# Kernel optimization log

Hardware: AMD Instinct MI355X
Metric: run time of the kernel (lower is better)

## Reference

```python
import jax, jax.numpy as jnp
import numpy as np

H, W, SCALE = 480, 640, 8  # full-res grid and coarse downsample factor (hw0_i/hw0_c)


def _struct_feats(pts, anchor_ids):
    """pts: [N, H*W, 3]; anchor_ids: [N, A] int -> [N, L, 4*A] with L=(H//SCALE)*(W//SCALE)."""
    N = pts.shape[0]
    coarse = pts.reshape(N, H, W, 3)[:, ::SCALE, ::SCALE, :].reshape(N, -1, 3)  # [N, L, 3]
    anchors = jnp.take_along_axis(pts, anchor_ids[:, :, None], axis=1)          # [N, A, 3]
    diff = coarse[:, :, None, :] - anchors[:, None, :, :]                        # [N, L, A, 3]
    dist = jnp.sum(diff * diff, axis=-1, keepdims=True)                          # [N, L, A, 1]
    s = jnp.concatenate([diff, dist], axis=-1)                                   # [N, L, A, 4]
    s = s / jnp.sum(jnp.abs(s), axis=-2, keepdims=True)                          # L1 norm over anchor axis
    s = jnp.swapaxes(s, -1, -2).reshape(N, coarse.shape[1], -1)                  # [N, L, 4A]
    return s


def _mlp(x, W1, b1, W2, b2):
    return jax.nn.relu(x @ W1 + b1) @ W2 + b2


def setup_inputs() -> dict:
    key = jax.random.key(0)
    ks = jax.random.split(key, 10)
    N, L, C, A, P = 4, 4800, 256, 128, H * W
    D = C + 4 * A  # 768
    return {
        "feat0": jax.random.normal(ks[0], (N, L, C), jnp.float32),
        "feat1": jax.random.normal(ks[1], (N, L, C), jnp.float32),
        "pts_3d0": jax.random.normal(ks[2], (N, P, 3), jnp.float32),
        "pts_3d1": jax.random.normal(ks[3], (N, P, 3), jnp.float32),
        "anchor_i_ids": jax.random.randint(ks[4], (N, A), 0, P),
        "anchor_j_ids": jax.random.randint(ks[5], (N, A), 0, P),
        "W1": jax.random.normal(ks[6], (D, D), jnp.float32) * (1.0 / np.sqrt(D)),
        "b1": jnp.zeros((D,), jnp.float32),
        "W2": jax.random.normal(ks[7], (D, C), jnp.float32) * (1.0 / np.sqrt(D)),
        "b2": jnp.zeros((C,), jnp.float32),
    }


def reference(feat0, feat1, pts_3d0, pts_3d1, anchor_i_ids, anchor_j_ids, W1, b1, W2, b2):
    s0 = _struct_feats(pts_3d0, anchor_i_ids)  # [N, L, 4A]
    s1 = _struct_feats(pts_3d1, anchor_j_ids)
    aug0 = _mlp(jnp.concatenate([feat0, s0], axis=-1), W1, b1, W2, b2)  # [N, L, C]
    aug1 = _mlp(jnp.concatenate([feat1, s1], axis=-1), W1, b1, W2, b2)
    return (aug0, aug1)
```

## Files before the change

kernel.cpp:

```cpp
#include <hip/hip_runtime.h>
#include <stdint.h>
#include <stddef.h>

typedef __attribute__((ext_vector_type(8))) short short8;
typedef __attribute__((ext_vector_type(4))) short short4v;
typedef __attribute__((ext_vector_type(4))) float f32x4;

typedef const __attribute__((address_space(3))) char* lds_cp;

#define GLDS16(gp, lp)                                                        \
    __builtin_amdgcn_global_load_lds(                                         \
        (const __attribute__((address_space(1))) void*)(gp),                  \
        (__attribute__((address_space(3))) void*)(lp), 16, 0, 0)

__device__ __forceinline__ short8 ldsr16(lds_cp p) {
    short8 v;
    asm volatile("ds_read_b128 %0, %1" : "=v"(v) : "v"(p));
    return v;
}

template <int N>
__device__ __forceinline__ void wait_lgkm() {
    static_assert(N == 0 || N == 2 || N == 4 || N == 8, "unsupported count");
    if constexpr (N == 0) asm volatile("s_waitcnt lgkmcnt(0)" ::: "memory");
    else if constexpr (N == 2) asm volatile("s_waitcnt lgkmcnt(2)" ::: "memory");
    else if constexpr (N == 4) asm volatile("s_waitcnt lgkmcnt(4)" ::: "memory");
    else if constexpr (N == 8) asm volatile("s_waitcnt lgkmcnt(8)" ::: "memory");
    __builtin_amdgcn_sched_barrier(0);
}

__device__ __forceinline__ unsigned short f2bf(float f) {
    union { float f; uint32_t u; } v;
    v.f = f;
    uint32_t u = v.u;
    u += 0x7FFFu + ((u >> 16) & 1u);
    return (unsigned short)(u >> 16);
}

__global__ __launch_bounds__(1024) void transpose_to_bf16(
    const float* __restrict__ src, unsigned short* __restrict__ dst, int R, int C)
{
    __shared__ float tile[32][33];
    const int c0 = blockIdx.x * 32, r0 = blockIdx.y * 32;
    const int tx = threadIdx.x, ty = threadIdx.y;
    tile[ty][tx] = src[(size_t)(r0 + ty) * C + (c0 + tx)];
    __syncthreads();
    dst[(size_t)(c0 + ty) * R + (r0 + tx)] = f2bf(tile[tx][ty]);
}

__global__ __launch_bounds__(64) void struct_pack(
    const float* __restrict__ feat0, const float* __restrict__ feat1,
    const float* __restrict__ pts0,  const float* __restrict__ pts1,
    const int* __restrict__ ids0,    const int* __restrict__ ids1,
    unsigned short* __restrict__ xw)
{
    const int m = blockIdx.x;
    const int t = m / 19200;
    const int r = m % 19200;
    const int n = r / 4800;
    const int l = r % 4800;
    const float* feat = t ? feat1 : feat0;
    const float* pts  = (t ? pts1 : pts0) + (size_t)n * (307200 * 3);
    const int*   ids  = (t ? ids1 : ids0) + n * 128;
    const int a = threadIdx.x;

    const int lr = l / 80, lc = l % 80;
    const int p  = (lr * 8) * 640 + lc * 8;
    const float cx = pts[p * 3 + 0], cy = pts[p * 3 + 1], cz = pts[p * 3 + 2];

    const int id0 = ids[a], id1 = ids[a + 64];
    const float d0x = cx - pts[id0 * 3 + 0];
    const float d0y = cy - pts[id0 * 3 + 1];
    const float d0z = cz - pts[id0 * 3 + 2];
    const float d0d = d0x * d0x + d0y * d0y + d0z * d0z;
    const float d1x = cx - pts[id1 * 3 + 0];
    const float d1y = cy - pts[id1 * 3 + 1];
    const float d1z = cz - pts[id1 * 3 + 2];
    const float d1d = d1x * d1x + d1y * d1y + d1z * d1z;

    float p0 = fabsf(d0x) + fabsf(d1x);
    float p1 = fabsf(d0y) + fabsf(d1y);
    float p2 = fabsf(d0z) + fabsf(d1z);
    float p3 = d0d + d1d;
#pragma unroll
    for (int off = 32; off; off >>= 1) {
        p0 += __shfl_xor(p0, off);
        p1 += __shfl_xor(p1, off);
        p2 += __shfl_xor(p2, off);
        p3 += __shfl_xor(p3, off);
    }
    const float i0 = 1.0f / p0, i1 = 1.0f / p1, i2 = 1.0f / p2, i3 = 1.0f / p3;

    unsigned short* xrow = xw + (size_t)m * 768;
    const float* frow = feat + (size_t)(n * 4800 + l) * 256;
    const float4 fv = ((const float4*)frow)[a];
    short4v s4;
    s4.x = (short)f2bf(fv.x); s4.y = (short)f2bf(fv.y);
    s4.z = (short)f2bf(fv.z); s4.w = (short)f2bf(fv.w);
    *(short4v*)(xrow + a * 4) = s4;

    xrow[256 + 0 * 128 + a]      = f2bf(d0x * i0);
    xrow[256 + 0 * 128 + a + 64] = f2bf(d1x * i0);
    xrow[256 + 1 * 128 + a]      = f2bf(d0y * i1);
    xrow[256 + 1 * 128 + a + 64] = f2bf(d1y * i1);
    xrow[256 + 2 * 128 + a]      = f2bf(d0z * i2);
    xrow[256 + 2 * 128 + a + 64] = f2bf(d1z * i2);
    xrow[256 + 3 * 128 + a]      = f2bf(d0d * i3);
    xrow[256 + 3 * 128 + a + 64] = f2bf(d1d * i3);
}

template <int MI, int NJ, int WRN_LOG, bool RELU, bool OUT_BF16>
__global__ __launch_bounds__(512, 2) void gemm_t(
    const unsigned short* __restrict__ A,
    const unsigned short* __restrict__ Bt,
    const float* __restrict__ bias,
    void* __restrict__ Cout,
    int K, int N, int ntx, int q8, int r8)
{
    constexpr int WRN = 1 << WRN_LOG;
    constexpr int WRM = 8 / WRN;
    constexpr int BM = WRM * MI * 16;
    constexpr int BN = WRN * NJ * 16;
    constexpr int ASLOT = BM * 128;
    constexpr int BSLOT = BN * 128;
    constexpr int ALD = BM / 64;
    constexpr int BLD = BN / 64;
    static_assert(ALD == 4, "vmcnt immediates assume 4 A-loads/wave/tile");
    static_assert(MI + NJ <= 13, "lgkm in-flight cap");

    extern __shared__ char lds[];
    const int nt = K >> 6;

    const int bid = blockIdx.x;
    const int xcd = bid & 7, idx = bid >> 3;
    const int w = (xcd < r8 ? xcd * (q8 + 1) : r8 * (q8 + 1) + (xcd - r8) * q8) + idx;
    const int n0 = (w % ntx) * BN;
    const int m0 = (w / ntx) * BM;

    const int tid = threadIdx.x;
    const int lane = tid & 63;
    const int wv = tid >> 6;
    const int wr = wv >> WRN_LOG;
    const int wc = wv & (WRN - 1);

    const int slr = lane >> 3;
    const int kc  = (lane & 7) ^ slr;
    const unsigned short* gA = A  + (size_t)(m0 + wv * 8 + slr) * K + kc * 8;
    const unsigned short* gB = Bt + (size_t)(n0 + wv * 8 + slr) * K + kc * 8;

    auto stA = [&](int slot, int i, int kt) {
        GLDS16(gA + (size_t)i * 64 * K + kt, lds + slot * ASLOT + (i * 64 + wv * 8) * 128);
    };
    auto stB = [&](int slot, int j, int kt) {
        GLDS16(gB + (size_t)j * 64 * K + kt, lds + 3 * ASLOT + slot * BSLOT + (j * 64 + wv * 8) * 128);
    };

    const int rsel = lane & 15;
    const int kbh  = lane >> 4;
    const int ck0 = ((kbh) ^ (rsel & 7)) * 16;
    const int ck1 = ((4 + kbh) ^ (rsel & 7)) * 16;
    const int aRowB = (wr * (MI * 16) + rsel) * 128;
    const int bRowB = (wc * (NJ * 16) + rsel) * 128;

    auto LDA = [&](int slot, int mi, int ks) -> short8 {
        return ldsr16((lds_cp)(lds + slot * ASLOT + aRowB + mi * 2048 + (ks ? ck1 : ck0)));
    };
    auto LDB = [&](int slot, int nj, int ks) -> short8 {
        return ldsr16((lds_cp)(lds + 3 * ASLOT + slot * BSLOT + bRowB + nj * 2048 + (ks ? ck1 : ck0)));
    };

    f32x4 acc[MI][NJ] = {};
    short8 aL[MI / 2], aH[MI / 2], aL1[MI / 2], aH1[MI / 2], bF0[NJ], bF1[NJ];

    {
#pragma unroll
        for (int i = 0; i < ALD; ++i) stA(0, i, 0);
#pragma unroll
        for (int j = 0; j < BLD; ++j) stB(0, j, 0);
        if (nt > 1) {
#pragma unroll
            for (int i = 0; i < ALD; ++i) stA(1, i, 64);
            asm volatile("s_waitcnt vmcnt(4)" ::: "memory");
        } else {
            asm volatile("s_waitcnt vmcnt(0)" ::: "memory");
        }
        __builtin_amdgcn_s_barrier();
    }

    int cb3 = 0;
    for (int t = 0; t < nt; ++t) {
        const int cb2 = t & 1;
        const int sb2 = cb2 ^ 1;
        int sa3 = cb3 + 2; if (sa3 >= 3) sa3 -= 3;
        const int kt1 = (t + 1) << 6;
        const int kt2 = (t + 2) << 6;
        const bool stb = (t + 1) < nt;
        const bool sta = (t + 2) < nt;

#pragma unroll
        for (int nj = 0; nj < NJ; ++nj) bF0[nj] = LDB(cb2, nj, 0);
#pragma unroll
        for (int mi = 0; mi < MI / 2; ++mi) aL[mi] = LDA(cb3, mi, 0);
#pragma unroll
        for (int mi = 0; mi < MI / 2; ++mi) aH[mi] = LDA(cb3, MI / 2 + mi, 0);

        wait_lgkm<MI / 2>();
        __builtin_amdgcn_s_setprio(1);
#pragma unroll
        for (int mi = 0; mi < MI / 2; ++mi)
#pragma unroll
            for (int nj = 0; nj < NJ; ++nj)
                acc[mi][nj] = __builtin_amdgcn_mfma_f32_16x16x32_bf16(aL[mi], bF0[nj], acc[mi][nj], 0, 0, 0);
        __builtin_amdgcn_s_setprio(0);

#pragma unroll
        for (int nj = 0; nj < NJ; ++nj) bF1[nj] = LDB(cb2, nj, 1);
        if (stb) {
#pragma unroll
            for (int j = 0; j < BLD; ++j) stB(sb2, j, kt1);
        }

        wait_lgkm<NJ>();
        __builtin_amdgcn_s_setprio(1);
#pragma unroll
        for (int mi = 0; mi < MI / 2; ++mi)
#pragma unroll
            for (int nj = 0; nj < NJ; ++nj)
                acc[MI / 2 + mi][nj] = __builtin_amdgcn_mfma_f32_16x16x32_bf16(aH[mi], bF0[nj], acc[MI / 2 + mi][nj], 0, 0, 0);
        __builtin_amdgcn_s_setprio(0);

#pragma unroll
        for (int mi = 0; mi < MI / 2; ++mi) aL1[mi] = LDA(cb3, mi, 1);
#pragma unroll
        for (int mi = 0; mi < MI / 2; ++mi) aH1[mi] = LDA(cb3, MI / 2 + mi, 1);
        if (sta) {
            stA(sa3, 0, kt2); stA(sa3, 1, kt2); stA(sa3, 2, kt2); stA(sa3, 3, kt2);
        }

        wait_lgkm<MI / 2>();
        __builtin_amdgcn_s_setprio(1);
#pragma unroll
        for (int mi = 0; mi < MI / 2; ++mi)
#pragma unroll
            for (int nj = 0; nj < NJ; ++nj)
                acc[mi][nj] = __builtin_amdgcn_mfma_f32_16x16x32_bf16(aL1[mi], bF1[nj], acc[mi][nj], 0, 0, 0);
        __builtin_amdgcn_s_setprio(0);

        wait_lgkm<0>();
        __builtin_amdgcn_s_setprio(1);
#pragma unroll
        for (int mi = 0; mi < MI / 2; ++mi)
#pragma unroll
            for (int nj = 0; nj < NJ; ++nj)
                acc[MI / 2 + mi][nj] = __builtin_amdgcn_mfma_f32_16x16x32_bf16(aH1[mi], bF1[nj], acc[MI / 2 + mi][nj], 0, 0, 0);
        __builtin_amdgcn_s_setprio(0);

        if (t + 1 < nt) {
            if (sta) asm volatile("s_waitcnt vmcnt(4)" ::: "memory");
            else     asm volatile("s_waitcnt vmcnt(0)" ::: "memory");
            __builtin_amdgcn_s_barrier();
        }
        cb3 = (cb3 + 1 == 3) ? 0 : cb3 + 1;
    }

    const int crow = (lane >> 4) * 4;
    const int ccol = lane & 15;
#pragma unroll
    for (int nj = 0; nj < NJ; ++nj) {
        const int col = n0 + wc * (NJ * 16) + nj * 16 + ccol;
        const float bv = bias[col];
#pragma unroll
        for (int mi = 0; mi < MI; ++mi) {
#pragma unroll
            for (int rg = 0; rg < 4; ++rg) {
                const int row = m0 + wr * (MI * 16) + mi * 16 + crow + rg;
                float v = acc[mi][nj][rg] + bv;
                if (RELU) v = fmaxf(v, 0.0f);
                if (OUT_BF16) {
                    ((unsigned short*)Cout)[(size_t)row * N + col] = f2bf(v);
                } else {
                    ((float*)Cout)[(size_t)row * N + col] = v;
                }
            }
        }
    }
}

extern "C" void kernel_launch(void* const* d_in, const int* in_sizes, int n_in,
                              void* d_out, int out_size, void* d_ws, size_t ws_size,
                              hipStream_t stream) {
    const float* feat0 = (const float*)d_in[0];
    const float* feat1 = (const float*)d_in[1];
    const float* pts0  = (const float*)d_in[2];
    const float* pts1  = (const float*)d_in[3];
    const int*   ids0  = (const int*)d_in[4];
    const int*   ids1  = (const int*)d_in[5];
    const float* W1    = (const float*)d_in[6];
    const float* b1    = (const float*)d_in[7];
    const float* W2    = (const float*)d_in[8];
    const float* b2    = (const float*)d_in[9];
    float* out = (float*)d_out;

    char* ws = (char*)d_ws;
    unsigned short* xw  = (unsigned short*)(ws);
    unsigned short* h   = (unsigned short*)(ws + 58982400);
    unsigned short* w1t = (unsigned short*)(ws + 117964800);
    unsigned short* w2t = (unsigned short*)(ws + 119144448);

    const int LDS1 = 3 * 32768 + 2 * 32768;
    const int LDS2 = 3 * 32768 + 2 * 16384;
    (void)hipFuncSetAttribute((const void*)&gemm_t<8, 4, 2, true, true>,
                              hipFuncAttributeMaxDynamicSharedMemorySize, LDS1);
    (void)hipFuncSetAttribute((const void*)&gemm_t<4, 4, 1, false, false>,
                              hipFuncAttributeMaxDynamicSharedMemorySize, LDS2);

    dim3 tb(32, 32);
    transpose_to_bf16<<<dim3(768 / 32, 768 / 32), tb, 0, stream>>>(W1, w1t, 768, 768);
    transpose_to_bf16<<<dim3(256 / 32, 768 / 32), tb, 0, stream>>>(W2, w2t, 768, 256);

    struct_pack<<<38400, 64, 0, stream>>>(feat0, feat1, pts0, pts1, ids0, ids1, xw);

    gemm_t<8, 4, 2, true, true><<<450, 512, LDS1, stream>>>(xw, w1t, b1, (void*)h, 768, 768, 3, 56, 2);
    gemm_t<4, 4, 1, false, false><<<300, 512, LDS2, stream>>>(h, w2t, b2, (void*)out, 768, 256, 2, 37, 4);
}
```

Baseline: 116.9 us.

## Merge weight transposes, batch struct_pack rows, shrink second GEMM tile

```diff
diff --git a/kernel.cpp b/kernel.cpp
--- a/kernel.cpp
+++ b/kernel.cpp
@@ -29,6 +29,14 @@
     __builtin_amdgcn_sched_barrier(0);
 }
 
+template <int N>
+__device__ __forceinline__ void wait_vm() {
+    static_assert(N == 0 || N == 2 || N == 4, "unsupported count");
+    if constexpr (N == 0) asm volatile("s_waitcnt vmcnt(0)" ::: "memory");
+    else if constexpr (N == 2) asm volatile("s_waitcnt vmcnt(2)" ::: "memory");
+    else if constexpr (N == 4) asm volatile("s_waitcnt vmcnt(4)" ::: "memory");
+}
+
 __device__ __forceinline__ unsigned short f2bf(float f) {
     union { float f; uint32_t u; } v;
     v.f = f;
@@ -37,24 +45,29 @@
     return (unsigned short)(u >> 16);
 }
 
-__global__ __launch_bounds__(1024) void transpose_to_bf16(
-    const float* __restrict__ src, unsigned short* __restrict__ dst, int R, int C)
+__global__ __launch_bounds__(1024) void transpose_w(
+    const float* __restrict__ W1, const float* __restrict__ W2,
+    unsigned short* __restrict__ w1t, unsigned short* __restrict__ w2t)
 {
     __shared__ float tile[32][33];
-    const int c0 = blockIdx.x * 32, r0 = blockIdx.y * 32;
+    int b = blockIdx.x;
+    const float* src; unsigned short* dst; int R, C, bx, by;
+    if (b < 576) { src = W1; dst = w1t; R = 768; C = 768; bx = b % 24; by = b / 24; }
+    else { b -= 576; src = W2; dst = w2t; R = 768; C = 256; bx = b % 8; by = b / 8; }
+    const int c0 = bx * 32, r0 = by * 32;
     const int tx = threadIdx.x, ty = threadIdx.y;
     tile[ty][tx] = src[(size_t)(r0 + ty) * C + (c0 + tx)];
     __syncthreads();
     dst[(size_t)(c0 + ty) * R + (r0 + tx)] = f2bf(tile[tx][ty]);
 }
 
-__global__ __launch_bounds__(64) void struct_pack(
+__global__ __launch_bounds__(256) void struct_pack(
     const float* __restrict__ feat0, const float* __restrict__ feat1,
     const float* __restrict__ pts0,  const float* __restrict__ pts1,
     const int* __restrict__ ids0,    const int* __restrict__ ids1,
     unsigned short* __restrict__ xw)
 {
-    const int m = blockIdx.x;
+    const int m = blockIdx.x * 4 + (threadIdx.x >> 6);
     const int t = m / 19200;
     const int r = m % 19200;
     const int n = r / 4800;
@@ -62,7 +75,7 @@
     const float* feat = t ? feat1 : feat0;
     const float* pts  = (t ? pts1 : pts0) + (size_t)n * (307200 * 3);
     const int*   ids  = (t ? ids1 : ids0) + n * 128;
-    const int a = threadIdx.x;
+    const int a = threadIdx.x & 63;
 
     const int lr = l / 80, lc = l % 80;
     const int p  = (lr * 8) * 640 + lc * 8;
@@ -125,10 +138,9 @@
     constexpr int BSLOT = BN * 128;
     constexpr int ALD = BM / 64;
     constexpr int BLD = BN / 64;
-    static_assert(ALD == 4, "vmcnt immediates assume 4 A-loads/wave/tile");
-    static_assert(MI + NJ <= 13, "lgkm in-flight cap");
 
     extern __shared__ char lds[];
+    char* ldsB = lds + 3 * ASLOT;
     const int nt = K >> 6;
 
     const int bid = blockIdx.x;
@@ -152,7 +164,7 @@
         GLDS16(gA + (size_t)i * 64 * K + kt, lds + slot * ASLOT + (i * 64 + wv * 8) * 128);
     };
     auto stB = [&](int slot, int j, int kt) {
-        GLDS16(gB + (size_t)j * 64 * K + kt, lds + 3 * ASLOT + slot * BSLOT + (j * 64 + wv * 8) * 128);
+        GLDS16(gB + (size_t)j * 64 * K + kt, ldsB + slot * BSLOT + (j * 64 + wv * 8) * 128);
     };
 
     const int rsel = lane & 15;
@@ -166,7 +178,7 @@
         return ldsr16((lds_cp)(lds + slot * ASLOT + aRowB + mi * 2048 + (ks ? ck1 : ck0)));
     };
     auto LDB = [&](int slot, int nj, int ks) -> short8 {
-        return ldsr16((lds_cp)(lds + 3 * ASLOT + slot * BSLOT + bRowB + nj * 2048 + (ks ? ck1 : ck0)));
+        return ldsr16((lds_cp)(ldsB + slot * BSLOT + bRowB + nj * 2048 + (ks ? ck1 : ck0)));
     };
 
     f32x4 acc[MI][NJ] = {};
@@ -180,9 +192,9 @@
         if (nt > 1) {
 #pragma unroll
             for (int i = 0; i < ALD; ++i) stA(1, i, 64);
-            asm volatile("s_waitcnt vmcnt(4)" ::: "memory");
+            wait_vm<ALD>();
         } else {
-            asm volatile("s_waitcnt vmcnt(0)" ::: "memory");
+            wait_vm<0>();
         }
         __builtin_amdgcn_s_barrier();
     }
@@ -234,7 +246,8 @@
 #pragma unroll
         for (int mi = 0; mi < MI / 2; ++mi) aH1[mi] = LDA(cb3, MI / 2 + mi, 1);
         if (sta) {
-            stA(sa3, 0, kt2); stA(sa3, 1, kt2); stA(sa3, 2, kt2); stA(sa3, 3, kt2);
+#pragma unroll
+            for (int i = 0; i < ALD; ++i) stA(sa3, i, kt2);
         }
 
         wait_lgkm<MI / 2>();
@@ -256,8 +269,8 @@
         __builtin_amdgcn_s_setprio(0);
 
         if (t + 1 < nt) {
-            if (sta) asm volatile("s_waitcnt vmcnt(4)" ::: "memory");
-            else     asm volatile("s_waitcnt vmcnt(0)" ::: "memory");
+            if (sta) wait_vm<ALD>();
+            else     wait_vm<0>();
             __builtin_amdgcn_s_barrier();
         }
         cb3 = (cb3 + 1 == 3) ? 0 : cb3 + 1;
@@ -308,18 +321,16 @@
     unsigned short* w2t = (unsigned short*)(ws + 119144448);
 
     const int LDS1 = 3 * 32768 + 2 * 32768;
-    const int LDS2 = 3 * 32768 + 2 * 16384;
+    const int LDS2 = 3 * 16384 + 2 * 16384;
     (void)hipFuncSetAttribute((const void*)&gemm_t<8, 4, 2, true, true>,
                               hipFuncAttributeMaxDynamicSharedMemorySize, LDS1);
-    (void)hipFuncSetAttribute((const void*)&gemm_t<4, 4, 1, false, false>,
+    (void)hipFuncSetAttribute((const void*)&gemm_t<4, 2, 2, false, false>,
                               hipFuncAttributeMaxDynamicSharedMemorySize, LDS2);
 
-    dim3 tb(32, 32);
-    transpose_to_bf16<<<dim3(768 / 32, 768 / 32), tb, 0, stream>>>(W1, w1t, 768, 768);
-    transpose_to_bf16<<<dim3(256 / 32, 768 / 32), tb, 0, stream>>>(W2, w2t, 768, 256);
-
-    struct_pack<<<38400, 64, 0, stream>>>(feat0, feat1, pts0, pts1, ids0, ids1, xw);
+    transpose_w<<<768, dim3(32, 32), 0, stream>>>(W1, W2, w1t, w2t);
+
+    struct_pack<<<9600, 256, 0, stream>>>(feat0, feat1, pts0, pts1, ids0, ids1, xw);
 
     gemm_t<8, 4, 2, true, true><<<450, 512, LDS1, stream>>>(xw, w1t, b1, (void*)h, 768, 768, 3, 56, 2);
-    gemm_t<4, 4, 1, false, false><<<300, 512, LDS2, stream>>>(h, w2t, b2, (void*)out, 768, 256, 2, 37, 4);
-}
+    gemm_t<4, 2, 2, false, false><<<600, 512, LDS2, stream>>>(h, w2t, b2, (void*)out, 768, 256, 2, 75, 0);
+}
```

After: 112.9 us. -3.4%, faster.
